# Kernel optimization log

Hardware: AMD Instinct MI355X
Metric: run time of the kernel (lower is better)

Reference implementation:

```python
import jax, jax.numpy as jnp
import numpy as np

EPS = 1e-5


def setup_inputs() -> dict:
    key = jax.random.key(0)
    k1, k2, k3 = jax.random.split(key, 3)
    B, D, T = 16, 256, 4096
    K = 2048
    x = jax.random.normal(k1, (B, D, T), dtype=jnp.float32)
    embedding_sum = jax.random.normal(k2, (K, D), dtype=jnp.float32)
    cluster_usage = jax.random.uniform(k3, (K,), dtype=jnp.float32)
    return {"x": x, "embedding_sum": embedding_sum, "cluster_usage": cluster_usage}


def reference(x, embedding_sum, cluster_usage):
    # embedding property: embedding_sum / clamp(cluster_usage, min=eps)
    emb = embedding_sum / jnp.clip(cluster_usage, EPS, None)[:, None]  # [K, D]
    B, D, T = x.shape
    x_flat = jnp.transpose(x, (0, 2, 1)).reshape(B * T, D)  # (b t) d
    # compute faithfully (clamped for numerical safety).
    x2 = jnp.sum(x_flat * x_flat, axis=-1, keepdims=True)      # [BT, 1]
    e2 = jnp.sum(emb * emb, axis=-1)                           # [K]
    d2 = x2 - 2.0 * (x_flat @ emb.T) + e2[None, :]             # [BT, K]
    distances = jnp.sqrt(jnp.clip(d2, 0.0, None))
    codes = jnp.argmin(distances, axis=-1).reshape(B, 1, T)    # int codes
    # decode: embedding gather, b t d -> b d t
    decoded = jnp.transpose(emb[codes[:, 0, :]], (0, 2, 1))    # [B, D, T]
    return codes, decoded
```

## Files before the change

### kernel.cpp

```cpp
#include <hip/hip_runtime.h>
#include <hip/hip_fp16.h>
#include <cmath>

#define EPS 1e-5f
#define TAU 0.15f
#define RP  8

#define Bn 16
#define Dn 256
#define Tn 4096
#define Kn 2048

typedef unsigned short ushort_t;
typedef __attribute__((ext_vector_type(8))) _Float16 f16x8;
typedef __attribute__((ext_vector_type(4))) float f32x4;

__device__ __forceinline__ unsigned short f2h(float v) {
    return __half_as_ushort(__float2half_rn(v));
}

__device__ __forceinline__ unsigned short f16_up(float v) {
    const __half h = __float2half_rn(v);
    const float back = __half2float(h);
    unsigned short u = __half_as_ushort(h);
    if (back < v) u = (u & 0x8000u) ? (u - 1) : (u + 1);
    return u;
}

#define GLOAD_LDS16(gp, lp) __builtin_amdgcn_global_load_lds( \
    (const __attribute__((address_space(1))) unsigned int*)(gp), \
    (__attribute__((address_space(3))) unsigned int*)(lp), 16, 0, 0)

__global__ __launch_bounds__(256) void prep_kernel(
    const float* __restrict__ es, const float* __restrict__ usage,
    float* __restrict__ emb, ushort_t* __restrict__ e16,
    float* __restrict__ bias, float4* __restrict__ embT4,
    int* __restrict__ counter)
{
    __shared__ float sh[256];
    __shared__ float wsum[4];
    const int k = blockIdx.x;
    const int d = threadIdx.x;
    const float inv = 1.0f / fmaxf(usage[k], EPS);
    const float v = es[(size_t)k * Dn + d] * inv;
    emb[(size_t)k * Dn + d] = v;
    e16[(size_t)k * Dn + d] = f2h(fminf(fmaxf(v, -65504.f), 65504.f));
    sh[d] = v;
    float sq = v * v;
    #pragma unroll
    for (int off = 32; off > 0; off >>= 1) sq += __shfl_down(sq, off, 64);
    const int lane = d & 63, wv = d >> 6;
    if (lane == 0) wsum[wv] = sq;
    __syncthreads();
    if (d < 64)
        embT4[(size_t)d * Kn + k] = make_float4(sh[4*d], sh[4*d+1], sh[4*d+2], sh[4*d+3]);
    if (d == 0) {
        bias[k] = 0.5f * (wsum[0] + wsum[1] + wsum[2] + wsum[3]);
        if (k == 0) *counter = 0;
    }
}

__global__ __launch_bounds__(256) void xsplit_kernel(
    const float* __restrict__ x, ushort_t* __restrict__ xh)
{
    __shared__ float tile[32 * 65];
    const int t0 = blockIdx.x * 64;
    const int d0 = blockIdx.y * 32;
    const int b  = blockIdx.z;
    const int tid = threadIdx.x;

    {
        const int dl = tid >> 3, tq = tid & 7;
        const float* src = x + ((size_t)(b * Dn + d0 + dl)) * Tn + t0 + tq * 8;
        const float4 a = *(const float4*)(src);
        const float4 c = *(const float4*)(src + 4);
        float* row = &tile[dl * 65 + tq * 8];
        row[0] = a.x; row[1] = a.y; row[2] = a.z; row[3] = a.w;
        row[4] = c.x; row[5] = c.y; row[6] = c.z; row[7] = c.w;
    }
    __syncthreads();
    {
        const int t_l = tid >> 2, dq = tid & 3;
        unsigned wh[4];
        #pragma unroll
        for (int i = 0; i < 4; ++i) {
            const float a = tile[(dq * 8 + 2 * i) * 65 + t_l];
            const float g = tile[(dq * 8 + 2 * i + 1) * 65 + t_l];
            wh[i] = (unsigned)f2h(a) | ((unsigned)f2h(g) << 16);
        }
        const size_t o = ((size_t)(b * Tn + t0 + t_l)) * Dn + d0 + dq * 8;
        *(uint4*)(xh + o) = make_uint4(wh[0], wh[1], wh[2], wh[3]);
    }
}

__global__ __launch_bounds__(256, 4) void gemm_argmax(
    const ushort_t* __restrict__ xh, const ushort_t* __restrict__ e16,
    const float* __restrict__ bias, uint2* __restrict__ rec)
{
    __shared__ ushort_t AhS[128 * 32];
    __shared__ ushort_t BhS[128 * 32];

    const int bid   = blockIdx.x;
    const int xcd   = bid & 7;
    const int ks    = (bid >> 3) & 7;
    const int tilid = bid >> 6;
    const int gtile = tilid * 8 + xcd;
    const int b     = gtile >> 5;
    const int tt    = gtile & 31;
    const int t0    = tt << 7;
    const int kbase = ks << 8;

    const int tid  = threadIdx.x;
    const int lane = tid & 63;
    const int wid  = tid >> 6;
    const int l15  = lane & 15;
    const int quad = lane >> 4;

    const size_t bTt0 = (size_t)b * Tn + t0;

    const int aoff0 = (wid * 32 + l15) * 32 + quad * 8;
    const int aoff1 = aoff0 + 16 * 32;
    const int boffL = l15 * 32 + quad * 8;

    float s1[8], s2[8];
    int   k1[8];
    #pragma unroll
    for (int rr = 0; rr < 8; ++rr) { s1[rr] = -INFINITY; s2[rr] = -INFINITY; k1[rr] = 0; }

    for (int kc = 0; kc < 2; ++kc) {
        const int k0 = kbase + kc * 128;

        f32x4 acc[2][8];
        #pragma unroll
        for (int i = 0; i < 2; ++i)
            #pragma unroll
            for (int j = 0; j < 8; ++j) acc[i][j] = (f32x4){0.f, 0.f, 0.f, 0.f};

        for (int dstep = 0; dstep < 8; ++dstep) {
            const int d0 = dstep * 32;
            __syncthreads();

            #pragma unroll
            for (int r = 0; r < 2; ++r) {
                const int cb = (r * 4 + wid) << 6;
                const int c  = cb + lane;
                const int row = c >> 2;
                const int doff = d0 + (c & 3) * 8;
                const size_t ao = (bTt0 + row) * Dn + doff;
                const size_t bo = ((size_t)(k0 + row)) * Dn + doff;
                const int lb = cb * 8;
                GLOAD_LDS16(xh + ao, AhS + lb);
                GLOAD_LDS16(e16 + bo, BhS + lb);
            }
            __syncthreads();

            const f16x8 ah0 = *(const f16x8*)(AhS + aoff0);
            const f16x8 ah1 = *(const f16x8*)(AhS + aoff1);
            #pragma unroll
            for (int j = 0; j < 8; ++j) {
                const f16x8 bh = *(const f16x8*)(BhS + (j << 9) + boffL);
                acc[0][j] = __builtin_amdgcn_mfma_f32_16x16x32_f16(ah0, bh, acc[0][j], 0, 0, 0);
                acc[1][j] = __builtin_amdgcn_mfma_f32_16x16x32_f16(ah1, bh, acc[1][j], 0, 0, 0);
            }
        }

        #pragma unroll
        for (int j = 0; j < 8; ++j) {
            const int kg = k0 + j * 16 + l15;
            const float bj = bias[kg];
            #pragma unroll
            for (int i = 0; i < 2; ++i) {
                #pragma unroll
                for (int r = 0; r < 4; ++r) {
                    const float s = acc[i][j][r] - bj;
                    const int rr = i * 4 + r;
                    if (s > s1[rr]) { s2[rr] = s1[rr]; s1[rr] = s; k1[rr] = kg; }
                    else if (s > s2[rr]) s2[rr] = s;
                }
            }
        }
    }

    #pragma unroll
    for (int m = 1; m <= 8; m <<= 1) {
        #pragma unroll
        for (int rr = 0; rr < 8; ++rr) {
            const float os1 = __shfl_xor(s1[rr], m);
            const float os2 = __shfl_xor(s2[rr], m);
            const int   ok1 = __shfl_xor(k1[rr], m);
            const bool take = (os1 > s1[rr]) || (os1 == s1[rr] && ok1 < k1[rr]);
            const float ns2 = take ? fmaxf(s1[rr], os2) : fmaxf(s2[rr], os1);
            if (take) { s1[rr] = os1; k1[rr] = ok1; }
            s2[rr] = ns2;
        }
    }

    if (l15 == 0) {
        #pragma unroll
        for (int rr = 0; rr < 8; ++rr) {
            const int i = rr >> 2, r = rr & 3;
            const int row = wid * 32 + i * 16 + quad * 4 + r;
            uint2 e;
            e.x = __float_as_uint(s1[rr]);
            e.y = ((unsigned)f16_up(s2[rr]) << 16) | (unsigned)k1[rr];
            rec[(size_t)ks * (Bn * Tn) + bTt0 + row] = e;
        }
    }
}

__global__ __launch_bounds__(256) void merge_kernel(
    const uint2* __restrict__ rec, int* __restrict__ codes_i,
    float* __restrict__ codes_f, int* __restrict__ list, int* __restrict__ counter)
{
    const int p = blockIdx.x * 256 + threadIdx.x;
    uint2 e = rec[p];
    float g1 = __uint_as_float(e.x);
    float g2 = __half2float(__ushort_as_half((unsigned short)(e.y >> 16)));
    int kk = (int)(e.y & 0xffffu);
    #pragma unroll
    for (int s = 1; s < 8; ++s) {
        e = rec[(size_t)s * (Bn * Tn) + p];
        const float s1 = __uint_as_float(e.x);
        if (s1 > g1) {
            const float s2u = __half2float(__ushort_as_half((unsigned short)(e.y >> 16)));
            g2 = fmaxf(fmaxf(g2, g1), s2u);
            g1 = s1;
            kk = (int)(e.y & 0xffffu);
        } else {
            g2 = fmaxf(g2, s1);
        }
    }
    codes_i[p] = kk;
    codes_f[p] = (float)kk;
    if (g1 - g2 < TAU) {
        const int idx = atomicAdd(counter, 1);
        list[idx] = p;
    }
}

__global__ __launch_bounds__(256) void rescue_kernel(
    const float* __restrict__ x, const float4* __restrict__ embT4,
    const float* __restrict__ bias, const int* __restrict__ list,
    const int* __restrict__ counter, int* __restrict__ codes_i,
    float* __restrict__ codes_f)
{
    __shared__ float xv[RP][256];
    __shared__ int plist[RP];
    __shared__ float rs[RP][4];
    __shared__ int   rk[RP][4];
    const int tid = threadIdx.x, lane = tid & 63, wid = tid >> 6;
    const int count = *counter;
    for (int base = blockIdx.x * RP; base < count; base += gridDim.x * RP) {
        const int npts = min(RP, count - base);
        __syncthreads();
        if (tid < npts) plist[tid] = list[base + tid];
        __syncthreads();
        for (int pi = 0; pi < npts; ++pi) {
            const int p = plist[pi];
            xv[pi][tid] = x[((size_t)((p >> 12) * Dn + tid)) * Tn + (p & 4095)];
        }
        for (int pi = npts; pi < RP; ++pi) xv[pi][tid] = 0.f;
        __syncthreads();

        float acc[8][RP];
        #pragma unroll
        for (int s = 0; s < 8; ++s)
            #pragma unroll
            for (int pi = 0; pi < RP; ++pi) acc[s][pi] = 0.f;

        for (int dc = 0; dc < 64; ++dc) {
            float4 ev[8];
            #pragma unroll
            for (int s = 0; s < 8; ++s)
                ev[s] = embT4[(size_t)dc * Kn + tid + (s << 8)];
            #pragma unroll
            for (int pi = 0; pi < RP; ++pi) {
                const float4 xw = *(const float4*)&xv[pi][dc << 2];
                #pragma unroll
                for (int s = 0; s < 8; ++s)
                    acc[s][pi] += ev[s].x * xw.x + ev[s].y * xw.y
                                + ev[s].z * xw.z + ev[s].w * xw.w;
            }
        }

        float bs[RP]; int bk[RP];
        #pragma unroll
        for (int pi = 0; pi < RP; ++pi) { bs[pi] = -INFINITY; bk[pi] = 0; }
        #pragma unroll
        for (int s = 0; s < 8; ++s) {
            const int kk = tid + (s << 8);
            const float bv = bias[kk];
            #pragma unroll
            for (int pi = 0; pi < RP; ++pi) {
                const float sc = acc[s][pi] - bv;
                if (sc > bs[pi]) { bs[pi] = sc; bk[pi] = kk; }
            }
        }
        #pragma unroll
        for (int off = 1; off < 64; off <<= 1) {
            #pragma unroll
            for (int pi = 0; pi < RP; ++pi) {
                const float os = __shfl_xor(bs[pi], off);
                const int   ok = __shfl_xor(bk[pi], off);
                if (os > bs[pi] || (os == bs[pi] && ok < bk[pi])) { bs[pi] = os; bk[pi] = ok; }
            }
        }
        if (lane == 0) {
            #pragma unroll
            for (int pi = 0; pi < RP; ++pi) { rs[pi][wid] = bs[pi]; rk[pi][wid] = bk[pi]; }
        }
        __syncthreads();
        if (tid < npts) {
            float fs = rs[tid][0]; int fk = rk[tid][0];
            #pragma unroll
            for (int w = 1; w < 4; ++w) {
                if (rs[tid][w] > fs || (rs[tid][w] == fs && rk[tid][w] < fk)) {
                    fs = rs[tid][w]; fk = rk[tid][w];
                }
            }
            const int p = plist[tid];
            codes_i[p] = fk;
            codes_f[p] = (float)fk;
        }
    }
}

__global__ __launch_bounds__(256) void decode_kernel(
    const float* __restrict__ emb, const int* __restrict__ codes,
    float* __restrict__ out)
{
    const int b = blockIdx.y;
    const int t = blockIdx.x * 256 + threadIdx.x;
    const int c = codes[(size_t)b * Tn + t];
    const float4* e4 = (const float4*)(emb + (size_t)c * Dn);
    float* ob = out + (size_t)b * Dn * Tn + t;
    #pragma unroll 4
    for (int d4 = 0; d4 < 64; ++d4) {
        const float4 v = e4[d4];
        ob[(size_t)(d4 * 4 + 0) * Tn] = v.x;
        ob[(size_t)(d4 * 4 + 1) * Tn] = v.y;
        ob[(size_t)(d4 * 4 + 2) * Tn] = v.z;
        ob[(size_t)(d4 * 4 + 3) * Tn] = v.w;
    }
}

extern "C" void kernel_launch(void* const* d_in, const int* in_sizes, int n_in,
                              void* d_out, int out_size, void* d_ws, size_t ws_size,
                              hipStream_t stream) {
    const float* x     = (const float*)d_in[0];
    const float* es    = (const float*)d_in[1];
    const float* usage = (const float*)d_in[2];

    char* ws = (char*)d_ws;
    float*    emb     = (float*)(ws + 0);
    float*    bias    = (float*)(ws + 2097152);
    ushort_t* e16     = (ushort_t*)(ws + 2105344);
    float4*   embT4   = (float4*)(ws + 3153920);
    int*      codes_i = (int*)(ws + 5251072);
    int*      list    = (int*)(ws + 5513216);
    int*      counter = (int*)(ws + 5775360);

    float* codes_f = (float*)d_out;
    float* decoded = (float*)d_out + (size_t)Bn * Tn;

    ushort_t* xh  = (ushort_t*)decoded;
    uint2*    rec = (uint2*)((char*)decoded + 33554432);

    prep_kernel<<<Kn, 256, 0, stream>>>(es, usage, emb, e16, bias, embT4, counter);

    dim3 gx(Tn / 64, Dn / 32, Bn);
    xsplit_kernel<<<gx, 256, 0, stream>>>(x, xh);

    gemm_argmax<<<4096, 256, 0, stream>>>(xh, e16, bias, rec);

    merge_kernel<<<(Bn * Tn) / 256, 256, 0, stream>>>(rec, codes_i, codes_f, list, counter);

    rescue_kernel<<<1024, 256, 0, stream>>>(x, embT4, bias, list, counter, codes_i, codes_f);

    dim3 g6(Tn / 256, Bn);
    decode_kernel<<<g6, 256, 0, stream>>>(emb, codes_i, decoded);
}
```

Baseline: 358.8 us.

## Enlarge GEMM-argmax tile to 256x256 with double-buffered swizzled LDS pipeline

Rewrites the distance GEMM kernel to use 512-thread blocks that each compute a 256(T)x256(K) tile with 8 waves each owning 64x128. A/B panels of 64 along D are staged into double-buffered XOR-swizzled LDS, so loads of the next panel overlap MFMA work on the current one, with s_setprio around the MFMA bursts. This raises arithmetic intensity and cuts LDS bank conflicts and barriers compared with the previous 128x128, d=32 single-buffer loop. The cost is a much larger LDS footprint and register use, and 16 partial-argmax slots instead of 8, which doubles the record traffic read by the merge kernel.

```diff
diff --git a/kernel.cpp b/kernel.cpp
--- a/kernel.cpp
+++ b/kernel.cpp
@@ -10,6 +10,7 @@
 #define Dn 256
 #define Tn 4096
 #define Kn 2048
+#define NSLOT 16
 
 typedef unsigned short ushort_t;
 typedef __attribute__((ext_vector_type(8))) _Float16 f16x8;
@@ -93,21 +94,64 @@
     }
 }
 
-__global__ __launch_bounds__(256, 4) void gemm_argmax(
+#define STAGE(q, d0)                                                          \
+    {                                                                         \
+        _Pragma("unroll")                                                     \
+        for (int r = 0; r < 4; ++r) {                                         \
+            const int cb = r * 512 + (wid << 6);                              \
+            GLOAD_LDS16(xh + (bTt0 + srow[r]) * Dn + (d0) + scol[r],          \
+                        &As[q][cb << 3]);                                     \
+        }                                                                     \
+        _Pragma("unroll")                                                     \
+        for (int r = 0; r < 4; ++r) {                                         \
+            const int cb = r * 512 + (wid << 6);                              \
+            GLOAD_LDS16(e16 + ((size_t)(kbase + srow[r])) * Dn + (d0) + scol[r], \
+                        &Bs[q][cb << 3]);                                     \
+        }                                                                     \
+    }
+
+#define COMPUTE(q)                                                            \
+    {                                                                         \
+        _Pragma("unroll")                                                     \
+        for (int sub = 0; sub < 2; ++sub) {                                   \
+            const int slot8 = ((((sub << 2) | quad) ^ x7) << 3);              \
+            f16x8 af[4]; f16x8 bf[8];                                         \
+            _Pragma("unroll")                                                 \
+            for (int i = 0; i < 4; ++i)                                       \
+                af[i] = *(const f16x8*)(&As[q][aoffbase + (i << 10) + slot8]);\
+            _Pragma("unroll")                                                 \
+            for (int j = 0; j < 8; ++j)                                       \
+                bf[j] = *(const f16x8*)(&Bs[q][boffbase + (j << 10) + slot8]);\
+            __builtin_amdgcn_s_setprio(1);                                    \
+            _Pragma("unroll")                                                 \
+            for (int i = 0; i < 4; ++i)                                       \
+                _Pragma("unroll")                                             \
+                for (int j = 0; j < 8; ++j)                                   \
+                    acc[i][j] = __builtin_amdgcn_mfma_f32_16x16x32_f16(       \
+                        af[i], bf[j], acc[i][j], 0, 0, 0);                    \
+            __builtin_amdgcn_s_setprio(0);                                    \
+        }                                                                     \
+    }
+
+#define BARRIER_PIN()                                                         \
+    __builtin_amdgcn_s_barrier();                                             \
+    __builtin_amdgcn_sched_barrier(0)
+
+__global__ __launch_bounds__(512, 2) void gemm_argmax(
     const ushort_t* __restrict__ xh, const ushort_t* __restrict__ e16,
     const float* __restrict__ bias, uint2* __restrict__ rec)
 {
-    __shared__ ushort_t AhS[128 * 32];
-    __shared__ ushort_t BhS[128 * 32];
+    __shared__ __align__(16) ushort_t As[2][256 * 64];
+    __shared__ __align__(16) ushort_t Bs[2][256 * 64];
 
     const int bid   = blockIdx.x;
     const int xcd   = bid & 7;
     const int ks    = (bid >> 3) & 7;
     const int tilid = bid >> 6;
     const int gtile = tilid * 8 + xcd;
-    const int b     = gtile >> 5;
-    const int tt    = gtile & 31;
-    const int t0    = tt << 7;
+    const int b     = gtile >> 4;
+    const int tt    = gtile & 15;
+    const int t0    = tt << 8;
     const int kbase = ks << 8;
 
     const int tid  = threadIdx.x;
@@ -115,95 +159,92 @@
     const int wid  = tid >> 6;
     const int l15  = lane & 15;
     const int quad = lane >> 4;
+    const int wm   = wid >> 1;
+    const int wn   = wid & 1;
+    const int x7   = l15 & 7;
 
     const size_t bTt0 = (size_t)b * Tn + t0;
 
-    const int aoff0 = (wid * 32 + l15) * 32 + quad * 8;
-    const int aoff1 = aoff0 + 16 * 32;
-    const int boffL = l15 * 32 + quad * 8;
-
-    float s1[8], s2[8];
-    int   k1[8];
-    #pragma unroll
-    for (int rr = 0; rr < 8; ++rr) { s1[rr] = -INFINITY; s2[rr] = -INFINITY; k1[rr] = 0; }
-
-    for (int kc = 0; kc < 2; ++kc) {
-        const int k0 = kbase + kc * 128;
-
-        f32x4 acc[2][8];
-        #pragma unroll
-        for (int i = 0; i < 2; ++i)
-            #pragma unroll
-            for (int j = 0; j < 8; ++j) acc[i][j] = (f32x4){0.f, 0.f, 0.f, 0.f};
-
-        for (int dstep = 0; dstep < 8; ++dstep) {
-            const int d0 = dstep * 32;
-            __syncthreads();
-
-            #pragma unroll
-            for (int r = 0; r < 2; ++r) {
-                const int cb = (r * 4 + wid) << 6;
-                const int c  = cb + lane;
-                const int row = c >> 2;
-                const int doff = d0 + (c & 3) * 8;
-                const size_t ao = (bTt0 + row) * Dn + doff;
-                const size_t bo = ((size_t)(k0 + row)) * Dn + doff;
-                const int lb = cb * 8;
-                GLOAD_LDS16(xh + ao, AhS + lb);
-                GLOAD_LDS16(e16 + bo, BhS + lb);
-            }
-            __syncthreads();
-
-            const f16x8 ah0 = *(const f16x8*)(AhS + aoff0);
-            const f16x8 ah1 = *(const f16x8*)(AhS + aoff1);
-            #pragma unroll
-            for (int j = 0; j < 8; ++j) {
-                const f16x8 bh = *(const f16x8*)(BhS + (j << 9) + boffL);
-                acc[0][j] = __builtin_amdgcn_mfma_f32_16x16x32_f16(ah0, bh, acc[0][j], 0, 0, 0);
-                acc[1][j] = __builtin_amdgcn_mfma_f32_16x16x32_f16(ah1, bh, acc[1][j], 0, 0, 0);
-            }
-        }
-
+    int srow[4], scol[4];
+    #pragma unroll
+    for (int r = 0; r < 4; ++r) {
+        const int c = r * 512 + tid;
+        srow[r] = c >> 3;
+        scol[r] = (((c & 7) ^ (srow[r] & 7)) << 3);
+    }
+
+    const int aoffbase = ((wm << 6) + l15) << 6;
+    const int boffbase = ((wn << 7) + l15) << 6;
+
+    f32x4 acc[4][8];
+    #pragma unroll
+    for (int i = 0; i < 4; ++i)
+        #pragma unroll
+        for (int j = 0; j < 8; ++j) acc[i][j] = (f32x4){0.f, 0.f, 0.f, 0.f};
+
+    STAGE(0, 0);
+    STAGE(1, 64);
+    asm volatile("s_waitcnt vmcnt(8)" ::: "memory");
+    BARRIER_PIN();
+    COMPUTE(0);
+    BARRIER_PIN();
+    STAGE(0, 128);
+    asm volatile("s_waitcnt vmcnt(8)" ::: "memory");
+    BARRIER_PIN();
+    COMPUTE(1);
+    BARRIER_PIN();
+    STAGE(1, 192);
+    asm volatile("s_waitcnt vmcnt(8)" ::: "memory");
+    BARRIER_PIN();
+    COMPUTE(0);
+    asm volatile("s_waitcnt vmcnt(0)" ::: "memory");
+    BARRIER_PIN();
+    COMPUTE(1);
+
+    __builtin_amdgcn_sched_barrier(0);
+    const int kw = kbase + (wn << 7);
+    float bj[8];
+    #pragma unroll
+    for (int j = 0; j < 8; ++j) bj[j] = bias[kw + (j << 4) + l15];
+
+    const int slot = (ks << 1) | wn;
+    #pragma unroll
+    for (int i = 0; i < 4; ++i) {
+        float s1[4], s2[4]; int k1[4];
+        #pragma unroll
+        for (int r = 0; r < 4; ++r) { s1[r] = -INFINITY; s2[r] = -INFINITY; k1[r] = 0; }
         #pragma unroll
         for (int j = 0; j < 8; ++j) {
-            const int kg = k0 + j * 16 + l15;
-            const float bj = bias[kg];
-            #pragma unroll
-            for (int i = 0; i < 2; ++i) {
-                #pragma unroll
-                for (int r = 0; r < 4; ++r) {
-                    const float s = acc[i][j][r] - bj;
-                    const int rr = i * 4 + r;
-                    if (s > s1[rr]) { s2[rr] = s1[rr]; s1[rr] = s; k1[rr] = kg; }
-                    else if (s > s2[rr]) s2[rr] = s;
-                }
-            }
-        }
-    }
-
-    #pragma unroll
-    for (int m = 1; m <= 8; m <<= 1) {
-        #pragma unroll
-        for (int rr = 0; rr < 8; ++rr) {
-            const float os1 = __shfl_xor(s1[rr], m);
-            const float os2 = __shfl_xor(s2[rr], m);
-            const int   ok1 = __shfl_xor(k1[rr], m);
-            const bool take = (os1 > s1[rr]) || (os1 == s1[rr] && ok1 < k1[rr]);
-            const float ns2 = take ? fmaxf(s1[rr], os2) : fmaxf(s2[rr], os1);
-            if (take) { s1[rr] = os1; k1[rr] = ok1; }
-            s2[rr] = ns2;
-        }
-    }
-
-    if (l15 == 0) {
-        #pragma unroll
-        for (int rr = 0; rr < 8; ++rr) {
-            const int i = rr >> 2, r = rr & 3;
-            const int row = wid * 32 + i * 16 + quad * 4 + r;
-            uint2 e;
-            e.x = __float_as_uint(s1[rr]);
-            e.y = ((unsigned)f16_up(s2[rr]) << 16) | (unsigned)k1[rr];
-            rec[(size_t)ks * (Bn * Tn) + bTt0 + row] = e;
+            const int kg = kw + (j << 4) + l15;
+            #pragma unroll
+            for (int r = 0; r < 4; ++r) {
+                const float s = acc[i][j][r] - bj[j];
+                if (s > s1[r]) { s2[r] = s1[r]; s1[r] = s; k1[r] = kg; }
+                else if (s > s2[r]) s2[r] = s;
+            }
+        }
+        #pragma unroll
+        for (int m = 1; m <= 8; m <<= 1) {
+            #pragma unroll
+            for (int r = 0; r < 4; ++r) {
+                const float os1 = __shfl_xor(s1[r], m);
+                const float os2 = __shfl_xor(s2[r], m);
+                const int   ok1 = __shfl_xor(k1[r], m);
+                const bool take = (os1 > s1[r]) || (os1 == s1[r] && ok1 < k1[r]);
+                const float ns2 = take ? fmaxf(s1[r], os2) : fmaxf(s2[r], os1);
+                if (take) { s1[r] = os1; k1[r] = ok1; }
+                s2[r] = ns2;
+            }
+        }
+        if (l15 == 0) {
+            #pragma unroll
+            for (int r = 0; r < 4; ++r) {
+                const int row = (wm << 6) + (i << 4) + (quad << 2) + r;
+                uint2 e;
+                e.x = __float_as_uint(s1[r]);
+                e.y = ((unsigned)f16_up(s2[r]) << 16) | (unsigned)k1[r];
+                rec[(size_t)slot * (Bn * Tn) + bTt0 + row] = e;
+            }
         }
     }
 }
@@ -218,7 +259,7 @@
     float g2 = __half2float(__ushort_as_half((unsigned short)(e.y >> 16)));
     int kk = (int)(e.y & 0xffffu);
     #pragma unroll
-    for (int s = 1; s < 8; ++s) {
+    for (int s = 1; s < NSLOT; ++s) {
         e = rec[(size_t)s * (Bn * Tn) + p];
         const float s1 = __uint_as_float(e.x);
         if (s1 > g1) {
@@ -371,7 +412,7 @@
     dim3 gx(Tn / 64, Dn / 32, Bn);
     xsplit_kernel<<<gx, 256, 0, stream>>>(x, xh);
 
-    gemm_argmax<<<4096, 256, 0, stream>>>(xh, e16, bias, rec);
+    gemm_argmax<<<2048, 512, 0, stream>>>(xh, e16, bias, rec);
 
     merge_kernel<<<(Bn * Tn) / 256, 256, 0, stream>>>(rec, codes_i, codes_f, list, counter);
 
```

Result: no change. 359.6 us (+0.2%).
